# Optimization experiments

Measured on AMD Instinct MI355X. Metric: run time of the kernel, lower is better.

The kernel has to match this reference:

```python
import jax, jax.numpy as jnp
import numpy as np
import math

N_NODES, CHANNELS, N_ELEM, N_FEAT = 4096, 128, 10, 128
LS_IN = [0, 1, 2]          # input irreps per channel: 0e+1o+2e -> dim 9
L_OUT = [0, 1]             # keep_irrep_out = {0e, 1o}
L12_MAX = 3                # cap on intermediate coupling
SLICES = {0: (0, 1), 1: (1, 4), 2: (4, 9)}
PATHS1 = [l for l in L_OUT if l in LS_IN]
PATHS2 = [(l1, l2, lo) for l1 in LS_IN for l2 in LS_IN for lo in L_OUT if abs(l1 - l2) <= lo <= l1 + l2]
T12_KEYS = [(l1, l2, l12) for l1 in LS_IN for l2 in LS_IN for l12 in range(abs(l1 - l2), min(l1 + l2, L12_MAX) + 1)]
PATHS3 = [(k, l3, lo) for k in T12_KEYS for l3 in LS_IN for lo in L_OUT if abs(k[2] - l3) <= lo <= k[2] + l3]

def _su2_cg(j1, m1, j2, m2, j3, m3):
    if m3 != m1 + m2:
        return 0.0
    f = math.factorial
    vmin = max(-j1 + j2 + m3, -j1 + m1, 0)
    vmax = min(j2 + j3 + m1, j3 - j1 + j2, j3 + m3)
    C = math.sqrt((2 * j3 + 1) * f(j3 + j1 - j2) * f(j3 - j1 + j2) * f(j1 + j2 - j3) * f(j3 + m3) * f(j3 - m3)
                  / (f(j1 + j2 + j3 + 1) * f(j1 - m1) * f(j1 + m1) * f(j2 - m2) * f(j2 + m2)))
    S = 0.0
    for v in range(vmin, vmax + 1):
        S += (-1) ** (v + j2 + m2) * f(j2 + j3 + m1 - v) * f(j1 - m1 + v) / (
            f(v) * f(j3 - j1 + j2 - v) * f(j3 + m3 - v) * f(v + j1 - j2 - m3))
    return C * S

def _c2r(l):
    # change of basis real -> complex spherical harmonics (e3nn convention)
    q = np.zeros((2 * l + 1, 2 * l + 1), dtype=np.complex128)
    for m in range(-l, 0):
        q[l + m, l + abs(m)] = 1.0 / math.sqrt(2)
        q[l + m, l - abs(m)] = -1j / math.sqrt(2)
    q[l, l] = 1.0
    for m in range(1, l + 1):
        q[l + m, l + abs(m)] = (-1) ** m / math.sqrt(2)
        q[l + m, l - abs(m)] = 1j * (-1) ** m / math.sqrt(2)
    return (-1j) ** l * q

_CG = {}
def real_cg(l1, l2, l3):
    key = (l1, l2, l3)
    if key not in _CG:
        Cc = np.zeros((2 * l1 + 1, 2 * l2 + 1, 2 * l3 + 1), dtype=np.complex128)
        for i, m1 in enumerate(range(-l1, l1 + 1)):
            for j, m2 in enumerate(range(-l2, l2 + 1)):
                for k, m3 in enumerate(range(-l3, l3 + 1)):
                    Cc[i, j, k] = _su2_cg(l1, m1, l2, m2, l3, m3)
        R = np.einsum('ij,kl,mn,ikn->jlm', _c2r(l1), _c2r(l2), np.conj(_c2r(l3).T), Cc)
        _CG[key] = np.real(R).astype(np.float32)
    return _CG[key]

def setup_inputs():
    key = jax.random.key(0)
    k = jax.random.split(key, 8)
    node_feats = jax.random.normal(k[0], (N_NODES, CHANNELS, 9), dtype=jnp.float32)
    species = jax.random.randint(k[1], (N_NODES,), 0, N_ELEM)
    w1 = jax.random.normal(k[2], (N_ELEM, len(PATHS1), CHANNELS), dtype=jnp.float32) / math.sqrt(len(PATHS1))
    w2 = jax.random.normal(k[3], (N_ELEM, len(PATHS2), CHANNELS), dtype=jnp.float32) / math.sqrt(len(PATHS2))
    w3 = jax.random.normal(k[4], (N_ELEM, len(PATHS3), CHANNELS), dtype=jnp.float32) / math.sqrt(len(PATHS3))
    lin_w0 = jax.random.normal(k[5], (CHANNELS, N_FEAT), dtype=jnp.float32)
    lin_w1 = jax.random.normal(k[6], (CHANNELS, N_FEAT), dtype=jnp.float32)
    return {"node_feats": node_feats, "w1": w1, "w2": w2, "w3": w3,
            "lin_w0": lin_w0, "lin_w1": lin_w1, "species": species}

def reference(node_feats, w1, w2, w3, lin_w0, lin_w1, species):
    n, c = node_feats.shape[:2]
    attrs = jax.nn.one_hot(species, N_ELEM, dtype=node_feats.dtype)
    A = {l: node_feats[..., SLICES[l][0]:SLICES[l][1]] for l in LS_IN}
    # element-dependent path weights per node
    w1n = jnp.einsum('ne,epc->npc', attrs, w1)
    w2n = jnp.einsum('ne,epc->npc', attrs, w2)
    w3n = jnp.einsum('ne,epc->npc', attrs, w3)
    B = {lo: jnp.zeros((n, c, 2 * lo + 1), node_feats.dtype) for lo in L_OUT}
    # correlation order 1
    for p, lo in enumerate(PATHS1):
        B[lo] = B[lo] + w1n[:, p, :, None] * A[lo]
    for p, (l1, l2, lo) in enumerate(PATHS2):
        cg = jnp.asarray(real_cg(l1, l2, lo))
        t = jnp.einsum('ijk,nci,ncj->nck', cg, A[l1], A[l2])
        B[lo] = B[lo] + w2n[:, p, :, None] * t
    T12 = {}
    for kk in T12_KEYS:
        l1, l2, l12 = kk
        T12[kk] = jnp.einsum('ijk,nci,ncj->nck', jnp.asarray(real_cg(l1, l2, l12)), A[l1], A[l2])
    for p, (kk, l3, lo) in enumerate(PATHS3):
        cg = jnp.asarray(real_cg(kk[2], l3, lo))
        t = jnp.einsum('ijk,nci,ncj->nck', cg, T12[kk], A[l3])
        B[lo] = B[lo] + w3n[:, p, :, None] * t
    # equivariant Linear: mix channel axis into num_features per output irrep
    s = 1.0 / math.sqrt(c)
    out0 = jnp.einsum('ncm,cf->nfm', B[0], lin_w0) * s
    out1 = jnp.einsum('ncm,cf->nfm', B[1], lin_w1) * s
    return jnp.concatenate([out0, out1], axis=-1)  # [N, F, 1+3]
```

## Files before the change

kernel.cpp:

```cpp
#include <hip/hip_runtime.h>
#include <utility>


#define NN 4096
#define NC 128
#define NE 10
#define TN 2

template<typename F, int... Is>
__device__ __forceinline__ void sfor_impl(F&& f, std::integer_sequence<int, Is...>) {
  (f(std::integral_constant<int, Is>{}), ...);
}
template<int N, typename F>
__device__ __forceinline__ void sfor(F&& f) {
  sfor_impl((F&&)f, std::make_integer_sequence<int, N>{});
}

constexpr int T_L1c[19]  = {0,0,0,1,1,1,1,1,1,1,2,2,2,2,2,2,2,2,3};
constexpr int T_L2c[19]  = {0,1,2,0,1,1,1,2,2,2,0,1,1,1,2,2,2,2,2};
constexpr int T_L3c[19]  = {0,1,2,1,0,1,2,1,2,3,2,1,2,3,0,1,2,3,1};
constexpr int T_OFFc[19] = {0,1,10,35,44,53,80,125,170,245,350,375,420,495,600,625,700,825,1000};
constexpr int AOFFc[3]   = {0,1,4};

constexpr int P2U_L1c[7]  = {0,0,1,1,1,2,2};
constexpr int P2U_L2c[7]  = {0,1,1,1,2,2,2};
constexpr int P2U_LOc[7]  = {0,1,0,1,1,0,1};
constexpr int P2U_TBLc[7] = {0,1,4,5,7,14,15};
constexpr int P2U_WAc[7]  = {0,1,3,4,5,7,8};
constexpr int P2U_WBc[7]  = {-1,2,-1,-1,6,-1,-1};

constexpr int K_L1c[18]  = {0,0,0,1,1,1,1,1,1,1,2,2,2,2,2,2,2,2};
constexpr int K_L2c[18]  = {0,1,2,0,1,1,1,2,2,2,0,1,1,1,2,2,2,2};
constexpr int K_L12c[18] = {0,1,2,1,0,1,2,1,2,3,2,1,2,3,0,1,2,3};

constexpr int   TT_CANONc[18] = {0,1,2,1,4,5,6,7,8,9,2,7,8,9,14,15,16,17};
constexpr float TT_SGNc[18]   = {1,1,1,1,1,1,1,1,1,1,1,1,-1,1,1,1,1,1};
constexpr int CANONc[13] = {0,1,2,4,5,6,7,8,9,14,15,16,17};
constexpr int CONS2c[13] = {-1,3,10,-1,-1,-1,11,12,13,-1,-1,-1,-1};

constexpr int P3_STARTc[19] = {0,2,6,9,13,15,19,22,26,29,30,33,37,40,41,43,47,50,51};
constexpr int P3_L3c[51] = {
  0,1,  0,1,1,2,  1,2,2,  0,1,1,2,  0,1,  0,1,1,2,  1,2,2,  0,1,1,2,  1,2,2,
  2,  1,2,2,  0,1,1,2,  1,2,2,  2,  0,1,  0,1,1,2,  1,2,2,  2 };
constexpr int P3_LOc[51] = {
  0,1,  1,0,1,1,  1,0,1,  1,0,1,1,  0,1,  1,0,1,1,  1,0,1,  1,0,1,1,  1,0,1,
  1,  1,0,1,  1,0,1,1,  1,0,1,  1,  0,1,  1,0,1,1,  1,0,1,  1 };
constexpr int P3_TBLc[51] = {
  0,1,  3,4,5,7,  11,14,15,  3,4,5,7,  0,1,  3,4,5,7,  11,14,15,  3,4,5,7,
  11,14,15,  18,  11,14,15,  3,4,5,7,  11,14,15,  18,  0,1,  3,4,5,7,
  11,14,15,  18 };

constexpr double cfact(int n) { double r = 1.0; for (int i = 2; i <= n; ++i) r *= i; return r; }
constexpr double csqrt(double x) {
  if (x <= 0.0) return 0.0;
  double r = x > 1.0 ? x : 1.0;
  for (int i = 0; i < 64; ++i) r = 0.5 * (r + x / r);
  return r;
}
constexpr double su2cg(int j1, int m1, int j2, int m2, int j3, int m3) {
  if (m3 != m1 + m2) return 0.0;
  int vmin = -j1 + j2 + m3; if (-j1 + m1 > vmin) vmin = -j1 + m1; if (vmin < 0) vmin = 0;
  int vmax = j2 + j3 + m1; if (j3 - j1 + j2 < vmax) vmax = j3 - j1 + j2; if (j3 + m3 < vmax) vmax = j3 + m3;
  double C = csqrt((2.0 * j3 + 1.0)
                   * cfact(j3 + j1 - j2) * cfact(j3 - j1 + j2) * cfact(j1 + j2 - j3)
                   * cfact(j3 + m3) * cfact(j3 - m3)
                   / (cfact(j1 + j2 + j3 + 1) * cfact(j1 - m1) * cfact(j1 + m1)
                      * cfact(j2 - m2) * cfact(j2 + m2)));
  double S = 0.0;
  for (int v = vmin; v <= vmax; ++v) {
    double sgn = ((v + j2 + m2) & 1) ? -1.0 : 1.0;
    S += sgn * cfact(j2 + j3 + m1 - v) * cfact(j1 - m1 + v)
         / (cfact(v) * cfact(j3 - j1 + j2 - v) * cfact(j3 + m3 - v) * cfact(v + j1 - j2 - m3));
  }
  return C * S;
}

struct Cx { double re, im; };
constexpr Cx cxmul(Cx a, Cx b) { return Cx{a.re * b.re - a.im * b.im, a.re * b.im + a.im * b.re}; }
struct Row { int cnt; int col[2]; Cx v[2]; };

constexpr Row c2r_row(int l, int r) {
  Row out{0, {0, 0}, {{0, 0}, {0, 0}}};
  constexpr double is2 = 0.70710678118654752440;
  const int m = r - l;
  if (m < 0) {
    out.cnt = 2;
    out.col[0] = l - m; out.v[0] = Cx{is2, 0.0};
    out.col[1] = l + m; out.v[1] = Cx{0.0, -is2};
  } else if (m == 0) {
    out.cnt = 1; out.col[0] = l; out.v[0] = Cx{1.0, 0.0};
  } else {
    const double sgn = (m & 1) ? -1.0 : 1.0;
    out.cnt = 2;
    out.col[0] = l + m; out.v[0] = Cx{sgn * is2, 0.0};
    out.col[1] = l - m; out.v[1] = Cx{0.0, sgn * is2};
  }
  const int ph = l & 3;
  for (int a = 0; a < out.cnt; ++a) {
    Cx v = out.v[a];
    out.v[a] = (ph == 0) ? v
             : (ph == 1) ? Cx{v.im, -v.re}
             : (ph == 2) ? Cx{-v.re, -v.im}
                         : Cx{-v.im, v.re};
  }
  return out;
}

struct CGAll { float v[1105]; };
constexpr CGAll make_cg() {
  CGAll R{};
  for (int t = 0; t < 19; ++t) {
    const int l1 = T_L1c[t], l2 = T_L2c[t], l3 = T_L3c[t], off = T_OFFc[t];
    const int d1 = 2 * l1 + 1, d2 = 2 * l2 + 1, d3 = 2 * l3 + 1;
    double tmp[175] = {};
    for (int i = 0; i < d1; ++i) {
      const int m1 = i - l1;
      const Row r1 = c2r_row(l1, i);
      for (int k = 0; k < d2; ++k) {
        const int m2 = k - l2, m3 = m1 + m2;
        if (m3 < -l3 || m3 > l3) continue;
        const double cc = su2cg(l1, m1, l2, m2, l3, m3);
        if (cc == 0.0) continue;
        const Row r2 = c2r_row(l2, k);
        const Row r3 = c2r_row(l3, m3 + l3);
        for (int a = 0; a < r1.cnt; ++a)
          for (int b = 0; b < r2.cnt; ++b) {
            const Cx q12 = cxmul(r1.v[a], r2.v[b]);
            for (int cdx = 0; cdx < r3.cnt; ++cdx) {
              const double re = q12.re * r3.v[cdx].re + q12.im * r3.v[cdx].im;
              tmp[(r1.col[a] * d2 + r2.col[b]) * d3 + r3.col[cdx]] += re * cc;
            }
          }
      }
    }
    const int sz = d1 * d2 * d3;
    for (int e = 0; e < sz; ++e) R.v[off + e] = (float)tmp[e];
  }
  return R;
}
constexpr CGAll CG_ALL = make_cg();

constexpr bool check_cg_sym() {
  for (int t = 0; t < 18; ++t) {
    const int tc = TT_CANONc[t];
    if (tc == t) continue;
    const int l1 = K_L1c[t], l2 = K_L2c[t], l12 = K_L12c[t];
    const int d1 = 2*l1+1, d2 = 2*l2+1, d12 = 2*l12+1;
    for (int i = 0; i < d1; ++i)
      for (int j = 0; j < d2; ++j)
        for (int k = 0; k < d12; ++k) {
          float a = CG_ALL.v[T_OFFc[t]  + (i*d2 + j)*d12 + k];
          float b = TT_SGNc[t] * CG_ALL.v[T_OFFc[tc] + (j*d1 + i)*d12 + k];
          float d = a - b; if (d < 0) d = -d;
          if (d > 1e-5f) return false;
        }
  }
  return true;
}
static_assert(check_cg_sym(), "CG exchange symmetry violated");

__global__ __launch_bounds__(256) void wt_pack(
    const float* __restrict__ w1, const float* __restrict__ w2,
    const float* __restrict__ w3, float4* __restrict__ wpack)
{
  const int tid = blockIdx.x * 256 + threadIdx.x;
  if (tid >= NE * 16 * NC) return;
  const int e = tid / (16 * NC);
  const int r = tid % (16 * NC);
  const int i = r / NC;
  const int c = r % NC;
  float v[4];
  #pragma unroll
  for (int j = 0; j < 4; ++j) {
    const int p = i * 4 + j;
    float x = 0.f;
    if (p < 2)       x = w1[((size_t)e * 2  + p)        * NC + c];
    else if (p < 11) x = w2[((size_t)e * 9  + (p - 2))  * NC + c];
    else if (p < 62) x = w3[((size_t)e * 51 + (p - 11)) * NC + c];
    v[j] = x;
  }
  wpack[tid] = make_float4(v[0], v[1], v[2], v[3]);
}

__global__ __launch_bounds__(256) void epb_main(
    const float*  __restrict__ nf,
    const float4* __restrict__ wpack,
    const float*  __restrict__ lw0,
    const float*  __restrict__ lw1,
    const int*    __restrict__ species,
    float* __restrict__ out)
{
  __shared__ float4 Bsh[TN * NC];
  __shared__ float4 psh[4 * TN * NC];
  const int t  = threadIdx.x;
  const int nb = blockIdx.x * TN;

  {
    const int c = t & 127, nl = t >> 7;
    const int s = species[nb + nl];

    float wr[64];
    {
      const float4* wp = wpack + ((size_t)s * 16) * NC + c;
      sfor<16>([&](auto I) {
        const float4 v = wp[I.value * NC];
        wr[4*I.value+0] = v.x; wr[4*I.value+1] = v.y;
        wr[4*I.value+2] = v.z; wr[4*I.value+3] = v.w;
      });
    }
    const float* ap = nf + ((size_t)(nb + nl) * NC + c) * 9;
    float A[9];
    sfor<9>([&](auto I) { A[I.value] = ap[I.value]; });

    float B[4];
    B[0] = wr[0] * A[0];
    B[1] = wr[1] * A[1];
    B[2] = wr[1] * A[2];
    B[3] = wr[1] * A[3];

    sfor<7>([&](auto P) {
      constexpr int p  = P.value;
      constexpr int l1 = P2U_L1c[p], l2 = P2U_L2c[p], lo = P2U_LOc[p];
      constexpr int d1 = 2*l1+1, d2 = 2*l2+1, dl = 2*lo+1;
      constexpr int off = T_OFFc[P2U_TBLc[p]];
      float w = wr[2 + P2U_WAc[p]];
      if constexpr (P2U_WBc[p] >= 0) w += wr[2 + P2U_WBc[p]];
      sfor<dl>([&](auto Kk) {
        constexpr int k = Kk.value;
        float v = 0.f;
        sfor<d1>([&](auto I) {
          sfor<d2>([&](auto J) {
            constexpr float cgc = CG_ALL.v[off + (I.value * d2 + J.value) * dl + k];
            if constexpr (cgc != 0.0f) {
              constexpr int ia = AOFFc[l1] + I.value, ja = AOFFc[l2] + J.value;
              constexpr int x = ia < ja ? ia : ja, y = ia < ja ? ja : ia;
              v = fmaf(cgc, A[x] * A[y], v);
            }
          });
        });
        B[lo + k] = fmaf(w, v, B[lo + k]);
      });
    });

    sfor<13>([&](auto CI) {
      constexpr int tk  = CANONc[CI.value];
      constexpr int l1  = K_L1c[tk], l2 = K_L2c[tk], l12 = K_L12c[tk];
      constexpr int d1  = 2*l1+1, d2 = 2*l2+1, d12 = 2*l12+1;
      constexpr int off = T_OFFc[tk];
      float tt[d12];
      sfor<d12>([&](auto Kk) {
        constexpr int k = Kk.value;
        float v = 0.f;
        sfor<d1>([&](auto I) {
          sfor<d2>([&](auto J) {
            constexpr float cgc = CG_ALL.v[off + (I.value * d2 + J.value) * d12 + k];
            if constexpr (cgc != 0.0f) {
              constexpr int ia = AOFFc[l1] + I.value, ja = AOFFc[l2] + J.value;
              constexpr int x = ia < ja ? ia : ja, y = ia < ja ? ja : ia;
              v = fmaf(cgc, A[x] * A[y], v);
            }
          });
        });
        tt[k] = v;
      });

      auto consume = [&](auto TK, auto SG) {
        constexpr int tkey = TK.value;
        constexpr float sgn = (float)SG.value;
        constexpr int pcnt = P3_STARTc[tkey + 1] - P3_STARTc[tkey];
        sfor<pcnt>([&](auto PP) {
          constexpr int p  = P3_STARTc[tkey] + PP.value;
          constexpr int l3 = P3_L3c[p], lo = P3_LOc[p];
          constexpr int d3 = 2*l3+1, dl = 2*lo+1;
          constexpr int off2 = T_OFFc[P3_TBLc[p]];
          const float w = wr[11 + p];
          sfor<dl>([&](auto M) {
            float v = 0.f;
            sfor<d12>([&](auto Kk) {
              sfor<d3>([&](auto J) {
                constexpr float cgc = sgn * CG_ALL.v[off2 + (Kk.value * d3 + J.value) * dl + M.value];
                if constexpr (cgc != 0.0f)
                  v = fmaf(cgc, tt[Kk.value] * A[AOFFc[l3] + J.value], v);
              });
            });
            B[lo + M.value] = fmaf(w, v, B[lo + M.value]);
          });
        });
      };
      consume(std::integral_constant<int, tk>{}, std::integral_constant<int, 1>{});
      constexpr int td = CONS2c[CI.value];
      if constexpr (td >= 0)
        consume(std::integral_constant<int, td>{},
                std::integral_constant<int, (int)TT_SGNc[td]>{});
    });

    Bsh[nl * NC + c] = make_float4(B[0], B[1], B[2], B[3]);
  }
  __syncthreads();

  {
    const int q  = t & 31;
    const int g  = (t >> 5) & 1;
    const int kp = t >> 6;
    const float4* pa4 = reinterpret_cast<const float4*>(lw0) + q;
    const float4* pb4 = reinterpret_cast<const float4*>(lw1) + q;
    const float4* bp  = &Bsh[g * NC + kp * 32];

    float4 of0{0,0,0,0}, of1{0,0,0,0}, of2{0,0,0,0}, of3{0,0,0,0};

    #pragma unroll 4
    for (int ch2 = 0; ch2 < 32; ++ch2) {
      const int ch = kp * 32 + ch2;
      const float4 wa = pa4[ch * 32];
      const float4 wb = pb4[ch * 32];
      const float4 b  = bp[ch2];
      of0.x = fmaf(b.x, wa.x, of0.x); of0.y = fmaf(b.y, wb.x, of0.y);
      of0.z = fmaf(b.z, wb.x, of0.z); of0.w = fmaf(b.w, wb.x, of0.w);
      of1.x = fmaf(b.x, wa.y, of1.x); of1.y = fmaf(b.y, wb.y, of1.y);
      of1.z = fmaf(b.z, wb.y, of1.z); of1.w = fmaf(b.w, wb.y, of1.w);
      of2.x = fmaf(b.x, wa.z, of2.x); of2.y = fmaf(b.y, wb.z, of2.y);
      of2.z = fmaf(b.z, wb.z, of2.z); of2.w = fmaf(b.w, wb.z, of2.w);
      of3.x = fmaf(b.x, wa.w, of3.x); of3.y = fmaf(b.y, wb.w, of3.y);
      of3.z = fmaf(b.z, wb.w, of3.z); of3.w = fmaf(b.w, wb.w, of3.w);
    }
    float4* pp = &psh[((kp * TN + g) * NC) + 4 * q];
    pp[0] = of0; pp[1] = of1; pp[2] = of2; pp[3] = of3;
  }
  __syncthreads();

  {
    const int f = t & 127, g2 = t >> 7;
    const float4 p0 = psh[((0 * TN + g2) * NC) + f];
    const float4 p1 = psh[((1 * TN + g2) * NC) + f];
    const float4 p2 = psh[((2 * TN + g2) * NC) + f];
    const float4 p3 = psh[((3 * TN + g2) * NC) + f];
    const float s4 = 0.08838834764831845f;
    float4 r;
    r.x = (p0.x + p1.x + p2.x + p3.x) * s4;
    r.y = (p0.y + p1.y + p2.y + p3.y) * s4;
    r.z = (p0.z + p1.z + p2.z + p3.z) * s4;
    r.w = (p0.w + p1.w + p2.w + p3.w) * s4;
    reinterpret_cast<float4*>(out)[(size_t)(nb + g2) * NC + f] = r;
  }
}

extern "C" void kernel_launch(void* const* d_in, const int* in_sizes, int n_in,
                              void* d_out, int out_size, void* d_ws, size_t ws_size,
                              hipStream_t stream) {
  const float* nf  = (const float*)d_in[0];
  const float* w1  = (const float*)d_in[1];
  const float* w2  = (const float*)d_in[2];
  const float* w3  = (const float*)d_in[3];
  const float* lw0 = (const float*)d_in[4];
  const float* lw1 = (const float*)d_in[5];
  const int*   spc = (const int*)  d_in[6];
  float* out = (float*)d_out;
  float4* wpack = (float4*)d_ws;
  (void)ws_size; (void)in_sizes; (void)n_in; (void)out_size;

  hipLaunchKernelGGL(wt_pack, dim3((NE * 16 * NC + 255) / 256), dim3(256), 0, stream,
                     w1, w2, w3, wpack);
  hipLaunchKernelGGL(epb_main, dim3(NN / TN), dim3(256), 0, stream,
                     nf, wpack, lw0, lw1, spc, out);
}
```

Baseline: 105.0 us.

## Split into basis and linear kernels with two-channel packed-FMA basis computation

Drops the weight-packing kernel and the fused single kernel. A new basis kernel computes two channels per thread with 2-wide vector FMAs, reading per-species weights straight from the input arrays, and writes the B tensor to workspace. A separate linear kernel handles 8 nodes per block with a full 128-channel loop per thread, which removes the partial-sum reduction in shared memory. The cost is a global-memory round trip for B and an extra kernel boundary.

```diff
diff --git a/kernel.cpp b/kernel.cpp
--- a/kernel.cpp
+++ b/kernel.cpp
@@ -5,7 +5,19 @@
 #define NN 4096
 #define NC 128
 #define NE 10
-#define TN 2
+
+typedef float v2f __attribute__((ext_vector_type(2)));
+
+__device__ __forceinline__ v2f ld2(const float* p) {
+  return *reinterpret_cast<const v2f*>(p);
+}
+__device__ __forceinline__ v2f cfma(float c, v2f x, v2f a) {
+  v2f cc = {c, c};
+  return __builtin_elementwise_fma(cc, x, a);
+}
+__device__ __forceinline__ v2f vfma(v2f w, v2f x, v2f a) {
+  return __builtin_elementwise_fma(w, x, a);
+}
 
 template<typename F, int... Is>
 __device__ __forceinline__ void sfor_impl(F&& f, std::integer_sequence<int, Is...>) {
@@ -159,189 +171,162 @@
 }
 static_assert(check_cg_sym(), "CG exchange symmetry violated");
 
-__global__ __launch_bounds__(256) void wt_pack(
-    const float* __restrict__ w1, const float* __restrict__ w2,
-    const float* __restrict__ w3, float4* __restrict__ wpack)
+__global__ __launch_bounds__(256) void epb_basis(
+    const float* __restrict__ nf,
+    const float* __restrict__ w1,
+    const float* __restrict__ w2,
+    const float* __restrict__ w3,
+    const int*   __restrict__ species,
+    float4* __restrict__ Bws)
 {
-  const int tid = blockIdx.x * 256 + threadIdx.x;
-  if (tid >= NE * 16 * NC) return;
-  const int e = tid / (16 * NC);
-  const int r = tid % (16 * NC);
-  const int i = r / NC;
-  const int c = r % NC;
-  float v[4];
-  #pragma unroll
-  for (int j = 0; j < 4; ++j) {
-    const int p = i * 4 + j;
-    float x = 0.f;
-    if (p < 2)       x = w1[((size_t)e * 2  + p)        * NC + c];
-    else if (p < 11) x = w2[((size_t)e * 9  + (p - 2))  * NC + c];
-    else if (p < 62) x = w3[((size_t)e * 51 + (p - 11)) * NC + c];
-    v[j] = x;
-  }
-  wpack[tid] = make_float4(v[0], v[1], v[2], v[3]);
-}
-
-__global__ __launch_bounds__(256) void epb_main(
-    const float*  __restrict__ nf,
-    const float4* __restrict__ wpack,
+  const int t  = threadIdx.x;
+  const int nb = blockIdx.x * 4;
+  const int nl = t >> 6;
+  const int c0 = (t & 63) * 2;
+  const int n  = nb + nl;
+  const int s  = species[n];
+
+  const float* ap = nf + ((size_t)n * NC + c0) * 9;
+  v2f A[9];
+  sfor<9>([&](auto I) { A[I.value] = v2f{ap[I.value], ap[I.value + 9]}; });
+
+  const float* w1p = w1 + (size_t)s * 2  * NC + c0;
+  const float* w2p = w2 + (size_t)s * 9  * NC + c0;
+  const float* w3p = w3 + (size_t)s * 51 * NC + c0;
+
+  v2f B[4];
+  {
+    const v2f wa = ld2(w1p), wb = ld2(w1p + NC);
+    B[0] = wa * A[0];
+    B[1] = wb * A[1];
+    B[2] = wb * A[2];
+    B[3] = wb * A[3];
+  }
+
+  sfor<7>([&](auto P) {
+    constexpr int p  = P.value;
+    constexpr int l1 = P2U_L1c[p], l2 = P2U_L2c[p], lo = P2U_LOc[p];
+    constexpr int d1 = 2*l1+1, d2 = 2*l2+1, dl = 2*lo+1;
+    constexpr int off = T_OFFc[P2U_TBLc[p]];
+    v2f w = ld2(w2p + P2U_WAc[p] * NC);
+    if constexpr (P2U_WBc[p] >= 0) w = w + ld2(w2p + P2U_WBc[p] * NC);
+    sfor<dl>([&](auto Kk) {
+      constexpr int k = Kk.value;
+      v2f v = {0.f, 0.f};
+      sfor<d1>([&](auto I) {
+        sfor<d2>([&](auto J) {
+          constexpr float cgc = CG_ALL.v[off + (I.value * d2 + J.value) * dl + k];
+          if constexpr (cgc != 0.0f) {
+            constexpr int ia = AOFFc[l1] + I.value, ja = AOFFc[l2] + J.value;
+            constexpr int x = ia < ja ? ia : ja, y = ia < ja ? ja : ia;
+            v = cfma(cgc, A[x] * A[y], v);
+          }
+        });
+      });
+      B[lo + k] = vfma(w, v, B[lo + k]);
+    });
+  });
+
+  sfor<13>([&](auto CI) {
+    constexpr int tk  = CANONc[CI.value];
+    constexpr int l1  = K_L1c[tk], l2 = K_L2c[tk], l12 = K_L12c[tk];
+    constexpr int d1  = 2*l1+1, d2 = 2*l2+1, d12 = 2*l12+1;
+    constexpr int off = T_OFFc[tk];
+    v2f tt[d12];
+    sfor<d12>([&](auto Kk) {
+      constexpr int k = Kk.value;
+      v2f v = {0.f, 0.f};
+      sfor<d1>([&](auto I) {
+        sfor<d2>([&](auto J) {
+          constexpr float cgc = CG_ALL.v[off + (I.value * d2 + J.value) * d12 + k];
+          if constexpr (cgc != 0.0f) {
+            constexpr int ia = AOFFc[l1] + I.value, ja = AOFFc[l2] + J.value;
+            constexpr int x = ia < ja ? ia : ja, y = ia < ja ? ja : ia;
+            v = cfma(cgc, A[x] * A[y], v);
+          }
+        });
+      });
+      tt[k] = v;
+    });
+
+    auto consume = [&](auto TK, auto SG) {
+      constexpr int tkey = TK.value;
+      constexpr float sgn = (float)SG.value;
+      constexpr int pcnt = P3_STARTc[tkey + 1] - P3_STARTc[tkey];
+      sfor<pcnt>([&](auto PP) {
+        constexpr int p  = P3_STARTc[tkey] + PP.value;
+        constexpr int l3 = P3_L3c[p], lo = P3_LOc[p];
+        constexpr int d3 = 2*l3+1, dl = 2*lo+1;
+        constexpr int off2 = T_OFFc[P3_TBLc[p]];
+        const v2f w = ld2(w3p + p * NC);
+        sfor<dl>([&](auto M) {
+          v2f v = {0.f, 0.f};
+          sfor<d12>([&](auto Kk) {
+            sfor<d3>([&](auto J) {
+              constexpr float cgc = sgn * CG_ALL.v[off2 + (Kk.value * d3 + J.value) * dl + M.value];
+              if constexpr (cgc != 0.0f)
+                v = cfma(cgc, tt[Kk.value] * A[AOFFc[l3] + J.value], v);
+            });
+          });
+          B[lo + M.value] = vfma(w, v, B[lo + M.value]);
+        });
+      });
+    };
+    consume(std::integral_constant<int, tk>{}, std::integral_constant<int, 1>{});
+    constexpr int td = CONS2c[CI.value];
+    if constexpr (td >= 0)
+      consume(std::integral_constant<int, td>{},
+              std::integral_constant<int, (int)TT_SGNc[td]>{});
+  });
+
+  Bws[(size_t)n * NC + c0]     = make_float4(B[0].x, B[1].x, B[2].x, B[3].x);
+  Bws[(size_t)n * NC + c0 + 1] = make_float4(B[0].y, B[1].y, B[2].y, B[3].y);
+}
+
+__global__ __launch_bounds__(256) void epb_linear(
+    const float4* __restrict__ Bws,
     const float*  __restrict__ lw0,
     const float*  __restrict__ lw1,
-    const int*    __restrict__ species,
     float* __restrict__ out)
 {
-  __shared__ float4 Bsh[TN * NC];
-  __shared__ float4 psh[4 * TN * NC];
+  __shared__ float4 Bsh[8 * NC];
   const int t  = threadIdx.x;
-  const int nb = blockIdx.x * TN;
-
-  {
-    const int c = t & 127, nl = t >> 7;
-    const int s = species[nb + nl];
-
-    float wr[64];
-    {
-      const float4* wp = wpack + ((size_t)s * 16) * NC + c;
-      sfor<16>([&](auto I) {
-        const float4 v = wp[I.value * NC];
-        wr[4*I.value+0] = v.x; wr[4*I.value+1] = v.y;
-        wr[4*I.value+2] = v.z; wr[4*I.value+3] = v.w;
-      });
-    }
-    const float* ap = nf + ((size_t)(nb + nl) * NC + c) * 9;
-    float A[9];
-    sfor<9>([&](auto I) { A[I.value] = ap[I.value]; });
-
-    float B[4];
-    B[0] = wr[0] * A[0];
-    B[1] = wr[1] * A[1];
-    B[2] = wr[1] * A[2];
-    B[3] = wr[1] * A[3];
-
-    sfor<7>([&](auto P) {
-      constexpr int p  = P.value;
-      constexpr int l1 = P2U_L1c[p], l2 = P2U_L2c[p], lo = P2U_LOc[p];
-      constexpr int d1 = 2*l1+1, d2 = 2*l2+1, dl = 2*lo+1;
-      constexpr int off = T_OFFc[P2U_TBLc[p]];
-      float w = wr[2 + P2U_WAc[p]];
-      if constexpr (P2U_WBc[p] >= 0) w += wr[2 + P2U_WBc[p]];
-      sfor<dl>([&](auto Kk) {
-        constexpr int k = Kk.value;
-        float v = 0.f;
-        sfor<d1>([&](auto I) {
-          sfor<d2>([&](auto J) {
-            constexpr float cgc = CG_ALL.v[off + (I.value * d2 + J.value) * dl + k];
-            if constexpr (cgc != 0.0f) {
-              constexpr int ia = AOFFc[l1] + I.value, ja = AOFFc[l2] + J.value;
-              constexpr int x = ia < ja ? ia : ja, y = ia < ja ? ja : ia;
-              v = fmaf(cgc, A[x] * A[y], v);
-            }
-          });
-        });
-        B[lo + k] = fmaf(w, v, B[lo + k]);
-      });
-    });
-
-    sfor<13>([&](auto CI) {
-      constexpr int tk  = CANONc[CI.value];
-      constexpr int l1  = K_L1c[tk], l2 = K_L2c[tk], l12 = K_L12c[tk];
-      constexpr int d1  = 2*l1+1, d2 = 2*l2+1, d12 = 2*l12+1;
-      constexpr int off = T_OFFc[tk];
-      float tt[d12];
-      sfor<d12>([&](auto Kk) {
-        constexpr int k = Kk.value;
-        float v = 0.f;
-        sfor<d1>([&](auto I) {
-          sfor<d2>([&](auto J) {
-            constexpr float cgc = CG_ALL.v[off + (I.value * d2 + J.value) * d12 + k];
-            if constexpr (cgc != 0.0f) {
-              constexpr int ia = AOFFc[l1] + I.value, ja = AOFFc[l2] + J.value;
-              constexpr int x = ia < ja ? ia : ja, y = ia < ja ? ja : ia;
-              v = fmaf(cgc, A[x] * A[y], v);
-            }
-          });
-        });
-        tt[k] = v;
-      });
-
-      auto consume = [&](auto TK, auto SG) {
-        constexpr int tkey = TK.value;
-        constexpr float sgn = (float)SG.value;
-        constexpr int pcnt = P3_STARTc[tkey + 1] - P3_STARTc[tkey];
-        sfor<pcnt>([&](auto PP) {
-          constexpr int p  = P3_STARTc[tkey] + PP.value;
-          constexpr int l3 = P3_L3c[p], lo = P3_LOc[p];
-          constexpr int d3 = 2*l3+1, dl = 2*lo+1;
-          constexpr int off2 = T_OFFc[P3_TBLc[p]];
-          const float w = wr[11 + p];
-          sfor<dl>([&](auto M) {
-            float v = 0.f;
-            sfor<d12>([&](auto Kk) {
-              sfor<d3>([&](auto J) {
-                constexpr float cgc = sgn * CG_ALL.v[off2 + (Kk.value * d3 + J.value) * dl + M.value];
-                if constexpr (cgc != 0.0f)
-                  v = fmaf(cgc, tt[Kk.value] * A[AOFFc[l3] + J.value], v);
-              });
-            });
-            B[lo + M.value] = fmaf(w, v, B[lo + M.value]);
-          });
-        });
-      };
-      consume(std::integral_constant<int, tk>{}, std::integral_constant<int, 1>{});
-      constexpr int td = CONS2c[CI.value];
-      if constexpr (td >= 0)
-        consume(std::integral_constant<int, td>{},
-                std::integral_constant<int, (int)TT_SGNc[td]>{});
-    });
-
-    Bsh[nl * NC + c] = make_float4(B[0], B[1], B[2], B[3]);
-  }
+  const int nb = blockIdx.x * 8;
+
+  const float4* src = Bws + (size_t)nb * NC;
+  #pragma unroll
+  for (int i = 0; i < 4; ++i) Bsh[t + 256 * i] = src[t + 256 * i];
   __syncthreads();
 
-  {
-    const int q  = t & 31;
-    const int g  = (t >> 5) & 1;
-    const int kp = t >> 6;
-    const float4* pa4 = reinterpret_cast<const float4*>(lw0) + q;
-    const float4* pb4 = reinterpret_cast<const float4*>(lw1) + q;
-    const float4* bp  = &Bsh[g * NC + kp * 32];
-
-    float4 of0{0,0,0,0}, of1{0,0,0,0}, of2{0,0,0,0}, of3{0,0,0,0};
-
-    #pragma unroll 4
-    for (int ch2 = 0; ch2 < 32; ++ch2) {
-      const int ch = kp * 32 + ch2;
-      const float4 wa = pa4[ch * 32];
-      const float4 wb = pb4[ch * 32];
-      const float4 b  = bp[ch2];
-      of0.x = fmaf(b.x, wa.x, of0.x); of0.y = fmaf(b.y, wb.x, of0.y);
-      of0.z = fmaf(b.z, wb.x, of0.z); of0.w = fmaf(b.w, wb.x, of0.w);
-      of1.x = fmaf(b.x, wa.y, of1.x); of1.y = fmaf(b.y, wb.y, of1.y);
-      of1.z = fmaf(b.z, wb.y, of1.z); of1.w = fmaf(b.w, wb.y, of1.w);
-      of2.x = fmaf(b.x, wa.z, of2.x); of2.y = fmaf(b.y, wb.z, of2.y);
-      of2.z = fmaf(b.z, wb.z, of2.z); of2.w = fmaf(b.w, wb.z, of2.w);
-      of3.x = fmaf(b.x, wa.w, of3.x); of3.y = fmaf(b.y, wb.w, of3.y);
-      of3.z = fmaf(b.z, wb.w, of3.z); of3.w = fmaf(b.w, wb.w, of3.w);
-    }
-    float4* pp = &psh[((kp * TN + g) * NC) + 4 * q];
-    pp[0] = of0; pp[1] = of1; pp[2] = of2; pp[3] = of3;
-  }
-  __syncthreads();
-
-  {
-    const int f = t & 127, g2 = t >> 7;
-    const float4 p0 = psh[((0 * TN + g2) * NC) + f];
-    const float4 p1 = psh[((1 * TN + g2) * NC) + f];
-    const float4 p2 = psh[((2 * TN + g2) * NC) + f];
-    const float4 p3 = psh[((3 * TN + g2) * NC) + f];
-    const float s4 = 0.08838834764831845f;
-    float4 r;
-    r.x = (p0.x + p1.x + p2.x + p3.x) * s4;
-    r.y = (p0.y + p1.y + p2.y + p3.y) * s4;
-    r.z = (p0.z + p1.z + p2.z + p3.z) * s4;
-    r.w = (p0.w + p1.w + p2.w + p3.w) * s4;
-    reinterpret_cast<float4*>(out)[(size_t)(nb + g2) * NC + f] = r;
-  }
+  const int q = t & 31;
+  const int g = t >> 5;
+  const float4* pa = reinterpret_cast<const float4*>(lw0) + q;
+  const float4* pb = reinterpret_cast<const float4*>(lw1) + q;
+  const float4* bp = &Bsh[g * NC];
+
+  float4 o0{0,0,0,0}, o1{0,0,0,0}, o2{0,0,0,0}, o3{0,0,0,0};
+
+  #pragma unroll 4
+  for (int ch = 0; ch < NC; ++ch) {
+    const float4 wa = pa[ch * 32];
+    const float4 wb = pb[ch * 32];
+    const float4 b  = bp[ch];
+    o0.x = fmaf(b.x, wa.x, o0.x); o0.y = fmaf(b.y, wb.x, o0.y);
+    o0.z = fmaf(b.z, wb.x, o0.z); o0.w = fmaf(b.w, wb.x, o0.w);
+    o1.x = fmaf(b.x, wa.y, o1.x); o1.y = fmaf(b.y, wb.y, o1.y);
+    o1.z = fmaf(b.z, wb.y, o1.z); o1.w = fmaf(b.w, wb.y, o1.w);
+    o2.x = fmaf(b.x, wa.z, o2.x); o2.y = fmaf(b.y, wb.z, o2.y);
+    o2.z = fmaf(b.z, wb.z, o2.z); o2.w = fmaf(b.w, wb.z, o2.w);
+    o3.x = fmaf(b.x, wa.w, o3.x); o3.y = fmaf(b.y, wb.w, o3.y);
+    o3.z = fmaf(b.z, wb.w, o3.z); o3.w = fmaf(b.w, wb.w, o3.w);
+  }
+
+  const float s4 = 0.08838834764831845f;
+  float4* out4 = reinterpret_cast<float4*>(out) + (size_t)(nb + g) * NC + 4 * q;
+  out4[0] = make_float4(o0.x*s4, o0.y*s4, o0.z*s4, o0.w*s4);
+  out4[1] = make_float4(o1.x*s4, o1.y*s4, o1.z*s4, o1.w*s4);
+  out4[2] = make_float4(o2.x*s4, o2.y*s4, o2.z*s4, o2.w*s4);
+  out4[3] = make_float4(o3.x*s4, o3.y*s4, o3.z*s4, o3.w*s4);
 }
 
 extern "C" void kernel_launch(void* const* d_in, const int* in_sizes, int n_in,
@@ -355,11 +340,11 @@
   const float* lw1 = (const float*)d_in[5];
   const int*   spc = (const int*)  d_in[6];
   float* out = (float*)d_out;
-  float4* wpack = (float4*)d_ws;
+  float4* Bws = (float4*)d_ws;
   (void)ws_size; (void)in_sizes; (void)n_in; (void)out_size;
 
-  hipLaunchKernelGGL(wt_pack, dim3((NE * 16 * NC + 255) / 256), dim3(256), 0, stream,
-                     w1, w2, w3, wpack);
-  hipLaunchKernelGGL(epb_main, dim3(NN / TN), dim3(256), 0, stream,
-                     nf, wpack, lw0, lw1, spc, out);
-}
+  hipLaunchKernelGGL(epb_basis, dim3(NN / 4), dim3(256), 0, stream,
+                     nf, w1, w2, w3, spc, Bws);
+  hipLaunchKernelGGL(epb_linear, dim3(NN / 8), dim3(256), 0, stream,
+                     Bws, lw0, lw1, out);
+}
```

Result: slower. 127.1 us (+21.0%).
